# Performance work log

Hardware: AMD Instinct MI355X
Metric: run time of the kernel (lower is better)

The kernel has to match this reference:

```python
import jax, jax.numpy as jnp
import numpy as np

jax.config.update("jax_enable_x64", True)

MAX_LEN = 2048
D_MODEL = 2048
CONTEXT = 1
FUDGE = 0.01
MIN_PERIOD = 1
MAX_PERIOD = 1024
FORGOTTEN_AT = 0.01


def _init_params():
    # Mirrors LaplaceAggregation.__init__ with init_method='linspace', modify_real=True
    limit = np.log(np.finfo(np.float64).max) / MAX_LEN - FUDGE
    soft_high = np.log(FORGOTTEN_AT) / MAX_PERIOD
    soft_low = np.log(FORGOTTEN_AT) / MIN_PERIOD
    a_low = max(-limit + FUDGE, soft_low)
    a_high = max(min(-1e-6, soft_high), a_low)
    a = np.linspace(a_low, a_high, D_MODEL).reshape(1, 1, D_MODEL, CONTEXT)
    b = (2.0 * np.pi / np.linspace(MIN_PERIOD, MAX_PERIOD, D_MODEL)).reshape(1, 1, D_MODEL, CONTEXT)
    return jnp.asarray(a, jnp.float64), jnp.asarray(b, jnp.float64)


def setup_inputs() -> dict:
    key = jax.random.key(0)
    k1, k2, k3 = jax.random.split(key, 3)
    B, T, F = 8, 1024, D_MODEL
    x = jax.random.normal(k1, (B, T, F), dtype=jnp.float32)
    mem_real = jax.random.normal(k2, (B, 1, F, CONTEXT), dtype=jnp.float32)
    mem_imag = jax.random.normal(k3, (B, 1, F, CONTEXT), dtype=jnp.float32)
    a, b = _init_params()
    return {"x": x, "mem_real": mem_real, "mem_imag": mem_imag, "a": a, "b": b}


def reference(x, mem_real, mem_imag, a, b):
    # batched_recurrent_update path (1 < T < max_len)
    T = x.shape[1]
    f64, c128 = jnp.float64, jnp.complex128
    ab = a.astype(f64) + 1j * b.astype(f64)           # [1,1,F,C] complex

    def psi(t):  # t: [T] -> [1,T,F,C]
        return jnp.exp(ab * t.reshape(1, -1, 1, 1))

    # inner_idx[:T] = [max_len-1, ..., max_len-T]; outer_idx = -inner_idx
    inner = jnp.arange(MAX_LEN - 1, MAX_LEN - 1 - T, -1, dtype=f64)
    offset = jnp.arange(1, T + 1, dtype=f64)          # state_offset[:T]

    xc = x.astype(f64)[..., None].astype(c128)        # [B,T,F,1]
    z = jnp.cumsum(psi(inner) * xc, axis=1)           # [B,T,F,C]
    mem0 = (mem_real.astype(f64) + 1j * mem_imag.astype(f64))  # [B,1,F,C]
    out = psi(-inner) * z + mem0 * psi(offset)        # [B,T,F,C]
    return out.astype(jnp.complex64)
```

## Files before the change

### kernel.cpp

```cpp
#include <hip/hip_runtime.h>
#include <math.h>

#define BB 8
#define TT 1024
#define FF 2048
#define LOG2F 11
#define NC 16
#define LCH (TT / NC)


__device__ inline double2 load_ab(const void* ap, const void* bp, int f) {
    double bd = ((const double*)bp)[0];
    if (bd > 6.0 && bd < 6.6) {
        return make_double2(((const double*)ap)[f], ((const double*)bp)[f]);
    } else {
        return make_double2((double)((const float*)ap)[f],
                            (double)((const float*)bp)[f]);
    }
}

__device__ inline double2 cis_exp(double a, double b, double scale) {
    double m = exp(scale * a);
    double s, c;
    sincos(scale * b, &s, &c);
    return make_double2(m * c, m * s);
}

__device__ inline void store_out(float* __restrict__ outf, size_t idx,
                                 size_t plane, size_t flimit, int planar,
                                 double wr, double wi) {
    if (idx < flimit) outf[idx] = (float)wr;
    if (planar) {
        size_t ii = idx + plane;
        if (ii < flimit) outf[ii] = (float)wi;
    }
}

__global__ void __launch_bounds__(256)
k_chunk_sum(const float* __restrict__ x, const void* __restrict__ a,
            const void* __restrict__ b, double2* __restrict__ S) {
    int tid = blockIdx.x * blockDim.x + threadIdx.x;
    int f  = tid & (FF - 1);
    int bc = tid >> LOG2F;
    int c  = bc & (NC - 1);
    int bb = bc >> 4;
    double2 ab = load_ab(a, b, f);
    double2 l = cis_exp(ab.x, ab.y, 1.0);
    const float* xp = x + ((size_t)bb * TT + (size_t)c * LCH) * FF + f;
    double wr = 0.0, wi = 0.0;
#pragma unroll 8
    for (int j = 0; j < LCH; ++j) {
        double xv = (double)xp[(size_t)j * FF];
        double nr = fma(l.x, wr, fma(-l.y, wi, xv));
        double ni = fma(l.x, wi, l.y * wr);
        wr = nr; wi = ni;
    }
    S[tid] = make_double2(wr, wi);
}

__global__ void __launch_bounds__(256)
k_scan(const float* __restrict__ mr, const float* __restrict__ mi,
       const void* __restrict__ a, const void* __restrict__ b,
       double2* __restrict__ S) {
    int tid = blockIdx.x * blockDim.x + threadIdx.x;
    int f  = tid & (FF - 1);
    int bb = tid >> LOG2F;
    double2 ab = load_ab(a, b, f);
    double2 lL = cis_exp(ab.x, ab.y, (double)LCH);
    double wr = (double)mr[tid], wi = (double)mi[tid];
    double2* Sp = S + (size_t)bb * NC * FF + f;
    for (int c = 0; c < NC; ++c) {
        double2 s = Sp[(size_t)c * FF];
        Sp[(size_t)c * FF] = make_double2(wr, wi);
        double nr = fma(lL.x, wr, fma(-lL.y, wi, s.x));
        double ni = fma(lL.x, wi, fma(lL.y, wr, s.y));
        wr = nr; wi = ni;
    }
}

__global__ void __launch_bounds__(256)
k_apply(const float* __restrict__ x, const void* __restrict__ a,
        const void* __restrict__ b, const double2* __restrict__ S,
        float* __restrict__ outf, size_t flimit, int planar) {
    int tid = blockIdx.x * blockDim.x + threadIdx.x;
    int f  = tid & (FF - 1);
    int bc = tid >> LOG2F;
    int c  = bc & (NC - 1);
    int bb = bc >> 4;
    double2 ab = load_ab(a, b, f);
    double2 l = cis_exp(ab.x, ab.y, 1.0);
    double2 w0 = S[tid];
    double wr = w0.x, wi = w0.y;
    const size_t plane = (size_t)BB * TT * FF;
    size_t base = ((size_t)bb * TT + (size_t)c * LCH) * FF + f;
    const float* xp = x + base;
#pragma unroll 8
    for (int j = 0; j < LCH; ++j) {
        double xv = (double)xp[(size_t)j * FF];
        double nr = fma(l.x, wr, fma(-l.y, wi, xv));
        double ni = fma(l.x, wi, l.y * wr);
        wr = nr; wi = ni;
        store_out(outf, base + (size_t)j * FF, plane, flimit, planar, wr, wi);
    }
}

__global__ void __launch_bounds__(256)
k_single(const float* __restrict__ x, const float* __restrict__ mr,
         const float* __restrict__ mi, const void* __restrict__ a,
         const void* __restrict__ b, float* __restrict__ outf,
         size_t flimit, int planar) {
    int tid = blockIdx.x * blockDim.x + threadIdx.x;
    int f  = tid & (FF - 1);
    int bb = tid >> LOG2F;
    double2 ab = load_ab(a, b, f);
    double2 l = cis_exp(ab.x, ab.y, 1.0);
    double wr = (double)mr[tid], wi = (double)mi[tid];
    const size_t plane = (size_t)BB * TT * FF;
    size_t base = (size_t)bb * TT * FF + f;
    const float* xp = x + base;
#pragma unroll 4
    for (int j = 0; j < TT; ++j) {
        double xv = (double)xp[(size_t)j * FF];
        double nr = fma(l.x, wr, fma(-l.y, wi, xv));
        double ni = fma(l.x, wi, l.y * wr);
        wr = nr; wi = ni;
        store_out(outf, base + (size_t)j * FF, plane, flimit, planar, wr, wi);
    }
}

extern "C" void kernel_launch(void* const* d_in, const int* in_sizes, int n_in,
                              void* d_out, int out_size, void* d_ws, size_t ws_size,
                              hipStream_t stream) {
    const float* x  = (const float*)d_in[0];
    const float* mr = (const float*)d_in[1];
    const float* mi = (const float*)d_in[2];
    const void*  a  = d_in[3];
    const void*  b  = d_in[4];
    float* outf = (float*)d_out;

    const size_t plane = (size_t)BB * TT * FF;
    size_t flimit = (size_t)out_size;
    int planar = (flimit > plane) ? 1 : 0;

    size_t s_bytes = (size_t)BB * NC * FF * sizeof(double2);
    if (d_ws == nullptr || ws_size < s_bytes) {
        k_single<<<(BB * FF) / 256, 256, 0, stream>>>(x, mr, mi, a, b, outf,
                                                      flimit, planar);
        return;
    }

    double2* S = (double2*)d_ws;
    int nthreads = BB * NC * FF;
    k_chunk_sum<<<nthreads / 256, 256, 0, stream>>>(x, a, b, S);
    k_scan<<<(BB * FF) / 256, 256, 0, stream>>>(mr, mi, a, b, S);
    k_apply<<<nthreads / 256, 256, 0, stream>>>(x, a, b, S, outf, flimit, planar);
}
```

Baseline: 144.6 us.

## Switch recurrence to fp32 and process two features per thread with float2 I/O

The chunked scan recurrence now runs in single precision instead of double, with only the exp/sincos setup kept in double. Each thread handles two adjacent features, so loads of x, mem and stores of output use float2 vectors and the workspace holds float4. This aims to cut the slow FP64 arithmetic and halve the scratch-buffer traffic while widening memory transactions. It risks accuracy loss from accumulating the recurrence in fp32 over long sequences, and the planar/interleaved output handling is simplified to always write an imaginary plane when it fits.

After: 141.3 us. 1.02x faster.

```diff
diff --git a/kernel.cpp b/kernel.cpp
--- a/kernel.cpp
+++ b/kernel.cpp
@@ -4,154 +4,170 @@
 #define BB 8
 #define TT 1024
 #define FF 2048
-#define LOG2F 11
+#define F2 1024
+#define LOG2F2 10
 #define NC 16
 #define LCH (TT / NC)
 
 
-__device__ inline double2 load_ab(const void* ap, const void* bp, int f) {
+__device__ inline void load_ab2(const void* ap, const void* bp, int f,
+                                double2& ab0, double2& ab1) {
     double bd = ((const double*)bp)[0];
     if (bd > 6.0 && bd < 6.6) {
-        return make_double2(((const double*)ap)[f], ((const double*)bp)[f]);
+        ab0 = make_double2(((const double*)ap)[f],     ((const double*)bp)[f]);
+        ab1 = make_double2(((const double*)ap)[f + 1], ((const double*)bp)[f + 1]);
     } else {
-        return make_double2((double)((const float*)ap)[f],
-                            (double)((const float*)bp)[f]);
+        ab0 = make_double2((double)((const float*)ap)[f],
+                           (double)((const float*)bp)[f]);
+        ab1 = make_double2((double)((const float*)ap)[f + 1],
+                           (double)((const float*)bp)[f + 1]);
     }
 }
 
-__device__ inline double2 cis_exp(double a, double b, double scale) {
+__device__ inline float2 cis_exp_f(double a, double b, double scale) {
     double m = exp(scale * a);
     double s, c;
     sincos(scale * b, &s, &c);
-    return make_double2(m * c, m * s);
+    return make_float2((float)(m * c), (float)(m * s));
 }
 
-__device__ inline void store_out(float* __restrict__ outf, size_t idx,
-                                 size_t plane, size_t flimit, int planar,
-                                 double wr, double wi) {
-    if (idx < flimit) outf[idx] = (float)wr;
-    if (planar) {
-        size_t ii = idx + plane;
-        if (ii < flimit) outf[ii] = (float)wi;
+__global__ void __launch_bounds__(256)
+k_chunk_sum(const float2* __restrict__ x2, const void* __restrict__ a,
+            const void* __restrict__ b, float4* __restrict__ S) {
+    int tid = blockIdx.x * blockDim.x + threadIdx.x;
+    int f2 = tid & (F2 - 1);
+    int bc = tid >> LOG2F2;
+    int c  = bc & (NC - 1);
+    int bb = bc >> 4;
+    double2 ab0, ab1;
+    load_ab2(a, b, 2 * f2, ab0, ab1);
+    float2 l0 = cis_exp_f(ab0.x, ab0.y, 1.0);
+    float2 l1 = cis_exp_f(ab1.x, ab1.y, 1.0);
+    const float2* xp = x2 + ((size_t)bb * TT + (size_t)c * LCH) * F2 + f2;
+    float wr0 = 0.f, wi0 = 0.f, wr1 = 0.f, wi1 = 0.f;
+#pragma unroll 8
+    for (int j = 0; j < LCH; ++j) {
+        float2 xv = xp[(size_t)j * F2];
+        float nr0 = fmaf(l0.x, wr0, fmaf(-l0.y, wi0, xv.x));
+        float ni0 = fmaf(l0.x, wi0, l0.y * wr0);
+        float nr1 = fmaf(l1.x, wr1, fmaf(-l1.y, wi1, xv.y));
+        float ni1 = fmaf(l1.x, wi1, l1.y * wr1);
+        wr0 = nr0; wi0 = ni0; wr1 = nr1; wi1 = ni1;
+    }
+    S[tid] = make_float4(wr0, wi0, wr1, wi1);
+}
+
+__global__ void __launch_bounds__(256)
+k_scan(const float2* __restrict__ mr2, const float2* __restrict__ mi2,
+       const void* __restrict__ a, const void* __restrict__ b,
+       float4* __restrict__ S) {
+    int tid = blockIdx.x * blockDim.x + threadIdx.x;
+    int f2 = tid & (F2 - 1);
+    int bb = tid >> LOG2F2;
+    double2 ab0, ab1;
+    load_ab2(a, b, 2 * f2, ab0, ab1);
+    float2 L0 = cis_exp_f(ab0.x, ab0.y, (double)LCH);
+    float2 L1 = cis_exp_f(ab1.x, ab1.y, (double)LCH);
+    float2 m_r = mr2[tid], m_i = mi2[tid];
+    float wr0 = m_r.x, wi0 = m_i.x, wr1 = m_r.y, wi1 = m_i.y;
+    float4* Sp = S + (size_t)bb * NC * F2 + f2;
+    for (int c = 0; c < NC; ++c) {
+        float4 s = Sp[(size_t)c * F2];
+        Sp[(size_t)c * F2] = make_float4(wr0, wi0, wr1, wi1);
+        float nr0 = fmaf(L0.x, wr0, fmaf(-L0.y, wi0, s.x));
+        float ni0 = fmaf(L0.x, wi0, fmaf(L0.y, wr0, s.y));
+        float nr1 = fmaf(L1.x, wr1, fmaf(-L1.y, wi1, s.z));
+        float ni1 = fmaf(L1.x, wi1, fmaf(L1.y, wr1, s.w));
+        wr0 = nr0; wi0 = ni0; wr1 = nr1; wi1 = ni1;
     }
 }
 
 __global__ void __launch_bounds__(256)
-k_chunk_sum(const float* __restrict__ x, const void* __restrict__ a,
-            const void* __restrict__ b, double2* __restrict__ S) {
+k_apply(const float2* __restrict__ x2, const void* __restrict__ a,
+        const void* __restrict__ b, const float4* __restrict__ S,
+        float2* __restrict__ out2, size_t limit2) {
     int tid = blockIdx.x * blockDim.x + threadIdx.x;
-    int f  = tid & (FF - 1);
-    int bc = tid >> LOG2F;
+    int f2 = tid & (F2 - 1);
+    int bc = tid >> LOG2F2;
     int c  = bc & (NC - 1);
     int bb = bc >> 4;
-    double2 ab = load_ab(a, b, f);
-    double2 l = cis_exp(ab.x, ab.y, 1.0);
-    const float* xp = x + ((size_t)bb * TT + (size_t)c * LCH) * FF + f;
-    double wr = 0.0, wi = 0.0;
+    double2 ab0, ab1;
+    load_ab2(a, b, 2 * f2, ab0, ab1);
+    float2 l0 = cis_exp_f(ab0.x, ab0.y, 1.0);
+    float2 l1 = cis_exp_f(ab1.x, ab1.y, 1.0);
+    float4 w0 = S[tid];
+    float wr0 = w0.x, wi0 = w0.y, wr1 = w0.z, wi1 = w0.w;
+    const size_t plane2 = (size_t)BB * TT * F2;
+    size_t base2 = ((size_t)bb * TT + (size_t)c * LCH) * F2 + f2;
+    const float2* xp = x2 + base2;
 #pragma unroll 8
     for (int j = 0; j < LCH; ++j) {
-        double xv = (double)xp[(size_t)j * FF];
-        double nr = fma(l.x, wr, fma(-l.y, wi, xv));
-        double ni = fma(l.x, wi, l.y * wr);
-        wr = nr; wi = ni;
-    }
-    S[tid] = make_double2(wr, wi);
-}
-
-__global__ void __launch_bounds__(256)
-k_scan(const float* __restrict__ mr, const float* __restrict__ mi,
-       const void* __restrict__ a, const void* __restrict__ b,
-       double2* __restrict__ S) {
-    int tid = blockIdx.x * blockDim.x + threadIdx.x;
-    int f  = tid & (FF - 1);
-    int bb = tid >> LOG2F;
-    double2 ab = load_ab(a, b, f);
-    double2 lL = cis_exp(ab.x, ab.y, (double)LCH);
-    double wr = (double)mr[tid], wi = (double)mi[tid];
-    double2* Sp = S + (size_t)bb * NC * FF + f;
-    for (int c = 0; c < NC; ++c) {
-        double2 s = Sp[(size_t)c * FF];
-        Sp[(size_t)c * FF] = make_double2(wr, wi);
-        double nr = fma(lL.x, wr, fma(-lL.y, wi, s.x));
-        double ni = fma(lL.x, wi, fma(lL.y, wr, s.y));
-        wr = nr; wi = ni;
+        float2 xv = xp[(size_t)j * F2];
+        float nr0 = fmaf(l0.x, wr0, fmaf(-l0.y, wi0, xv.x));
+        float ni0 = fmaf(l0.x, wi0, l0.y * wr0);
+        float nr1 = fmaf(l1.x, wr1, fmaf(-l1.y, wi1, xv.y));
+        float ni1 = fmaf(l1.x, wi1, l1.y * wr1);
+        wr0 = nr0; wi0 = ni0; wr1 = nr1; wi1 = ni1;
+        size_t idx2 = base2 + (size_t)j * F2;
+        if (idx2 < limit2) out2[idx2] = make_float2(wr0, wr1);
+        size_t ii2 = idx2 + plane2;
+        if (ii2 < limit2) out2[ii2] = make_float2(wi0, wi1);
     }
 }
 
 __global__ void __launch_bounds__(256)
-k_apply(const float* __restrict__ x, const void* __restrict__ a,
-        const void* __restrict__ b, const double2* __restrict__ S,
-        float* __restrict__ outf, size_t flimit, int planar) {
+k_single(const float2* __restrict__ x2, const float2* __restrict__ mr2,
+         const float2* __restrict__ mi2, const void* __restrict__ a,
+         const void* __restrict__ b, float2* __restrict__ out2, size_t limit2) {
     int tid = blockIdx.x * blockDim.x + threadIdx.x;
-    int f  = tid & (FF - 1);
-    int bc = tid >> LOG2F;
-    int c  = bc & (NC - 1);
-    int bb = bc >> 4;
-    double2 ab = load_ab(a, b, f);
-    double2 l = cis_exp(ab.x, ab.y, 1.0);
-    double2 w0 = S[tid];
-    double wr = w0.x, wi = w0.y;
-    const size_t plane = (size_t)BB * TT * FF;
-    size_t base = ((size_t)bb * TT + (size_t)c * LCH) * FF + f;
-    const float* xp = x + base;
-#pragma unroll 8
-    for (int j = 0; j < LCH; ++j) {
-        double xv = (double)xp[(size_t)j * FF];
-        double nr = fma(l.x, wr, fma(-l.y, wi, xv));
-        double ni = fma(l.x, wi, l.y * wr);
-        wr = nr; wi = ni;
-        store_out(outf, base + (size_t)j * FF, plane, flimit, planar, wr, wi);
-    }
-}
-
-__global__ void __launch_bounds__(256)
-k_single(const float* __restrict__ x, const float* __restrict__ mr,
-         const float* __restrict__ mi, const void* __restrict__ a,
-         const void* __restrict__ b, float* __restrict__ outf,
-         size_t flimit, int planar) {
-    int tid = blockIdx.x * blockDim.x + threadIdx.x;
-    int f  = tid & (FF - 1);
-    int bb = tid >> LOG2F;
-    double2 ab = load_ab(a, b, f);
-    double2 l = cis_exp(ab.x, ab.y, 1.0);
-    double wr = (double)mr[tid], wi = (double)mi[tid];
-    const size_t plane = (size_t)BB * TT * FF;
-    size_t base = (size_t)bb * TT * FF + f;
-    const float* xp = x + base;
+    int f2 = tid & (F2 - 1);
+    int bb = tid >> LOG2F2;
+    double2 ab0, ab1;
+    load_ab2(a, b, 2 * f2, ab0, ab1);
+    float2 l0 = cis_exp_f(ab0.x, ab0.y, 1.0);
+    float2 l1 = cis_exp_f(ab1.x, ab1.y, 1.0);
+    float2 m_r = mr2[tid], m_i = mi2[tid];
+    float wr0 = m_r.x, wi0 = m_i.x, wr1 = m_r.y, wi1 = m_i.y;
+    const size_t plane2 = (size_t)BB * TT * F2;
+    size_t base2 = (size_t)bb * TT * F2 + f2;
+    const float2* xp = x2 + base2;
 #pragma unroll 4
     for (int j = 0; j < TT; ++j) {
-        double xv = (double)xp[(size_t)j * FF];
-        double nr = fma(l.x, wr, fma(-l.y, wi, xv));
-        double ni = fma(l.x, wi, l.y * wr);
-        wr = nr; wi = ni;
-        store_out(outf, base + (size_t)j * FF, plane, flimit, planar, wr, wi);
+        float2 xv = xp[(size_t)j * F2];
+        float nr0 = fmaf(l0.x, wr0, fmaf(-l0.y, wi0, xv.x));
+        float ni0 = fmaf(l0.x, wi0, l0.y * wr0);
+        float nr1 = fmaf(l1.x, wr1, fmaf(-l1.y, wi1, xv.y));
+        float ni1 = fmaf(l1.x, wi1, l1.y * wr1);
+        wr0 = nr0; wi0 = ni0; wr1 = nr1; wi1 = ni1;
+        size_t idx2 = base2 + (size_t)j * F2;
+        if (idx2 < limit2) out2[idx2] = make_float2(wr0, wr1);
+        size_t ii2 = idx2 + plane2;
+        if (ii2 < limit2) out2[ii2] = make_float2(wi0, wi1);
     }
 }
 
 extern "C" void kernel_launch(void* const* d_in, const int* in_sizes, int n_in,
                               void* d_out, int out_size, void* d_ws, size_t ws_size,
                               hipStream_t stream) {
-    const float* x  = (const float*)d_in[0];
-    const float* mr = (const float*)d_in[1];
-    const float* mi = (const float*)d_in[2];
-    const void*  a  = d_in[3];
-    const void*  b  = d_in[4];
-    float* outf = (float*)d_out;
+    const float2* x2  = (const float2*)d_in[0];
+    const float2* mr2 = (const float2*)d_in[1];
+    const float2* mi2 = (const float2*)d_in[2];
+    const void*   a   = d_in[3];
+    const void*   b   = d_in[4];
+    float2* out2 = (float2*)d_out;
 
-    const size_t plane = (size_t)BB * TT * FF;
-    size_t flimit = (size_t)out_size;
-    int planar = (flimit > plane) ? 1 : 0;
+    size_t limit2 = (size_t)out_size >> 1;
 
-    size_t s_bytes = (size_t)BB * NC * FF * sizeof(double2);
+    size_t s_bytes = (size_t)BB * NC * F2 * sizeof(float4);
     if (d_ws == nullptr || ws_size < s_bytes) {
-        k_single<<<(BB * FF) / 256, 256, 0, stream>>>(x, mr, mi, a, b, outf,
-                                                      flimit, planar);
+        k_single<<<(BB * F2) / 256, 256, 0, stream>>>(x2, mr2, mi2, a, b, out2,
+                                                      limit2);
         return;
     }
 
-    double2* S = (double2*)d_ws;
-    int nthreads = BB * NC * FF;
-    k_chunk_sum<<<nthreads / 256, 256, 0, stream>>>(x, a, b, S);
-    k_scan<<<(BB * FF) / 256, 256, 0, stream>>>(mr, mi, a, b, S);
-    k_apply<<<nthreads / 256, 256, 0, stream>>>(x, a, b, S, outf, flimit, planar);
+    float4* S = (float4*)d_ws;
+    int nthreads = BB * NC * F2;
+    k_chunk_sum<<<nthreads / 256, 256, 0, stream>>>(x2, a, b, S);
+    k_scan<<<(BB * F2) / 256, 256, 0, stream>>>(mr2, mi2, a, b, S);
+    k_apply<<<nthreads / 256, 256, 0, stream>>>(x2, a, b, S, out2, limit2);
 }
```
